# Performance work log

Hardware: AMD Instinct MI355X
Metric: run time of the kernel (lower is better)

## Reference

```python
import jax, jax.numpy as jnp
import numpy as np

FIELD_DIMS = [100000, 1000, 100, 50]
NUM_FEATURES = 12
NUM_CAT = len(FIELD_DIMS)
NUM_CONT = NUM_FEATURES - NUM_CAT
D = 32            # embed_dim
HID = [64, 32]
B, T = 1024, 200
BN_EPS = 1e-5


def setup_inputs() -> dict:
    key = jax.random.key(0)
    ks = jax.random.split(key, 32)
    # x: [B, T, F]; first NUM_CAT cols are integer category ids stored as float
    cat_cols = [jax.random.randint(ks[i], (B, T, 1), 0, FIELD_DIMS[i]).astype(jnp.float32)
                for i in range(NUM_CAT)]
    cont_cols = jax.random.normal(ks[4], (B, T, NUM_CONT), dtype=jnp.float32)
    x = jnp.concatenate(cat_cols + [cont_cols], axis=-1)
    s = 0.05
    inp = {"x": x}
    for i, fd in enumerate(FIELD_DIMS):
        inp[f"emb{i}"] = jax.random.normal(ks[5 + i], (fd, D), dtype=jnp.float32) * s
        inp[f"lin{i}"] = jax.random.normal(ks[9 + i], (fd, D), dtype=jnp.float32) * s
    # Conv1d(1, D, 1) per continuous field == per-field affine map scalar -> D
    inp["cont_w"]  = jax.random.normal(ks[13], (NUM_CONT, D), dtype=jnp.float32) * s
    inp["cont_b"]  = jax.random.normal(ks[14], (NUM_CONT, D), dtype=jnp.float32) * s
    inp["clin_w"]  = jax.random.normal(ks[15], (NUM_CONT, D), dtype=jnp.float32) * s
    inp["clin_b"]  = jax.random.normal(ks[16], (NUM_CONT, D), dtype=jnp.float32) * s
    inp["fin_bias"] = jnp.zeros((D,), dtype=jnp.float32)
    # DNN tower: kernel_size-1 Conv1d == dense over channel dim
    dims = [NUM_FEATURES * D] + HID
    for li in range(len(HID)):
        fan_in = dims[li]
        inp[f"w{li+1}"] = jax.random.normal(ks[17 + 4 * li], (HID[li], fan_in), dtype=jnp.float32) / np.sqrt(fan_in)
        inp[f"b{li+1}"] = jnp.zeros((HID[li],), dtype=jnp.float32)
        inp[f"g{li+1}"] = jnp.ones((HID[li],), dtype=jnp.float32)
        inp[f"beta{li+1}"] = jnp.zeros((HID[li],), dtype=jnp.float32)
    inp["w_out"] = jax.random.normal(ks[30], (D, HID[-1]), dtype=jnp.float32) / np.sqrt(HID[-1])
    inp["b_out"] = jnp.zeros((D,), dtype=jnp.float32)
    return inp


def _batchnorm(h, g, b):
    # training-mode BN over (batch, time), biased variance (torch default)
    mu = h.mean(axis=(0, 1))
    var = h.var(axis=(0, 1))
    return g * (h - mu) * jax.lax.rsqrt(var + BN_EPS) + b


def reference(x, emb0, emb1, emb2, emb3, lin0, lin1, lin2, lin3,
              cont_w, cont_b, clin_w, clin_b, fin_bias,
              w1, b1, g1, beta1, w2, b2, g2, beta2, w_out, b_out):
    embs = [emb0, emb1, emb2, emb3]
    lins = [lin0, lin1, lin2, lin3]
    cat_idx = x[..., :NUM_CAT].astype(jnp.int32)          # [B,T,C]
    xc = x[..., NUM_CAT:]                                  # [B,T,Nc]

    # per-field embeddings -> [B,T,F,D]
    cat_emb = jnp.stack([embs[i][cat_idx[..., i]] for i in range(NUM_CAT)], axis=2)
    cont_emb = xc[..., None] * cont_w + cont_b             # [B,T,Nc,D]
    emb_all = jnp.concatenate([cat_emb, cont_emb], axis=2)  # [B,T,F,D]

    # FM pairwise interaction (sum-of-squares trick)
    s = emb_all.sum(axis=2)                                # [B,T,D]
    interaction = 0.5 * (s * s - (emb_all * emb_all).sum(axis=2))

    # linear terms
    lin_cat = sum(lins[i][cat_idx[..., i]] for i in range(NUM_CAT))      # [B,T,D]
    lin_cont = (xc[..., None] * clin_w + clin_b).sum(axis=2)             # [B,T,D]
    linear = lin_cat + lin_cont + fin_bias

    # DNN tower (k=1 convs == dense over F*D channels); dropout omitted (eval)
    h = emb_all.reshape(B, T, NUM_FEATURES * D)
    h = jax.nn.relu(_batchnorm(h @ w1.T + b1, g1, beta1))
    h = jax.nn.relu(_batchnorm(h @ w2.T + b2, g2, beta2))
    dnn = h @ w_out.T + b_out                              # [B,T,D]

    return linear + interaction + dnn                      # [B,T,D]
```

## Files before the change

### kernel.cpp

```cpp
#include <hip/hip_runtime.h>
#include <hip/hip_bf16.h>

typedef __hip_bfloat16 bf16;

#define ROWS 204800
#define N_INV (1.0f / 204800.0f)

__device__ float g_stats[256];
__device__ bf16  g_E1_0b[100000 * 64];
__device__ float g_E1_1[1000 * 64];
__device__ float g_E1_2[100 * 64];
__device__ float g_E1_3[50 * 64];
__device__ float g_U[8 * 64];
__device__ float g_Vb[64];
__device__ bf16  g_h1p[ROWS * 64];
__device__ bf16  g_h2p[ROWS * 32];
__device__ bf16  g_fmp[ROWS * 32];

__device__ __forceinline__ int clampi(int v, int hi) {
    return v < 0 ? 0 : (v > hi ? hi : v);
}
__device__ __forceinline__ float rl_f(float v, int l) {
    return __uint_as_float((unsigned int)__builtin_amdgcn_readlane((int)__float_as_uint(v), l));
}
__device__ __forceinline__ float us2f(unsigned short u) {
    return __uint_as_float(((unsigned int)u) << 16);
}

__device__ __forceinline__ int swz8(int d) {
    return (d & ~7) | ((d & 7) ^ ((d >> 3) & 7));
}
__device__ __forceinline__ int swz4(int d) {
    return (d & ~3) | ((d & 3) ^ (((d >> 2) ^ (d >> 4)) & 3));
}

#define GLOAD16(gp, lp)                                                        \
    __builtin_amdgcn_global_load_lds(                                          \
        (const __attribute__((address_space(1))) unsigned int*)(gp),           \
        (__attribute__((address_space(3))) unsigned int*)(lp), 16, 0, 0)

__global__ __launch_bounds__(64) void precompute_kernel(
    const float* __restrict__ emb1, const float* __restrict__ emb2, const float* __restrict__ emb3,
    const float* __restrict__ cont_w, const float* __restrict__ cont_b,
    const float* __restrict__ w1, const float* __restrict__ b1)
{
    int b = blockIdx.x;
    int k = threadIdx.x;
    __shared__ float row[32];

    if (b < 1150) {
        const float* tab; float* out; int i, colOff;
        if (b < 1000)      { tab = emb1; out = g_E1_1; i = b;        colOff = 32; }
        else if (b < 1100) { tab = emb2; out = g_E1_2; i = b - 1000; colOff = 64; }
        else               { tab = emb3; out = g_E1_3; i = b - 1100; colOff = 96; }
        if (k < 32) row[k] = tab[i * 32 + k];
        __syncthreads();
        const float* wr = w1 + k * 384 + colOff;
        float acc = 0.f;
        #pragma unroll
        for (int d = 0; d < 32; ++d) acc = fmaf(row[d], wr[d], acc);
        out[i * 64 + k] = acc;
    } else {
        g_stats[k]       = 0.f;
        g_stats[k + 64]  = 0.f;
        g_stats[k + 128] = 0.f;
        g_stats[k + 192] = 0.f;

        float vb = b1[k];
        #pragma unroll
        for (int j = 0; j < 8; ++j) {
            const float* wr = w1 + k * 384 + (4 + j) * 32;
            float u = 0.f;
            #pragma unroll
            for (int d = 0; d < 32; ++d) {
                float w = wr[d];
                u  = fmaf(cont_w[j * 32 + d], w, u);
                vb = fmaf(cont_b[j * 32 + d], w, vb);
            }
            g_U[j * 64 + k] = u;
        }
        g_Vb[k] = vb;
    }
}

__global__ __launch_bounds__(256) void e10_kernel(
    const float* __restrict__ emb0, const float* __restrict__ w1)
{
    int lane = threadIdx.x & 63;
    int wv   = threadIdx.x >> 6;
    int h    = lane >> 5;

    float w1col[32];
    {
        const float4* wr = (const float4*)(w1 + lane * 384);
        #pragma unroll
        for (int q = 0; q < 8; ++q) {
            float4 v = wr[q];
            w1col[4*q+0] = v.x; w1col[4*q+1] = v.y;
            w1col[4*q+2] = v.z; w1col[4*q+3] = v.w;
        }
    }

    for (int i = blockIdx.x * 8 + wv * 2; i < 100000; i += gridDim.x * 8) {
        int iA = i, iB = i + 1;
        float e = emb0[(h ? iB : iA) * 32 + (lane & 31)];

        float a0 = 0.f, a1 = 0.f, a2 = 0.f, a3 = 0.f;
        float b0 = 0.f, b1v = 0.f, b2v = 0.f, b3 = 0.f;
        #pragma unroll
        for (int dd = 0; dd < 32; dd += 4) {
            a0  = fmaf(rl_f(e, dd + 0),      w1col[dd + 0], a0);
            a1  = fmaf(rl_f(e, dd + 1),      w1col[dd + 1], a1);
            a2  = fmaf(rl_f(e, dd + 2),      w1col[dd + 2], a2);
            a3  = fmaf(rl_f(e, dd + 3),      w1col[dd + 3], a3);
            b0  = fmaf(rl_f(e, 32 + dd + 0), w1col[dd + 0], b0);
            b1v = fmaf(rl_f(e, 32 + dd + 1), w1col[dd + 1], b1v);
            b2v = fmaf(rl_f(e, 32 + dd + 2), w1col[dd + 2], b2v);
            b3  = fmaf(rl_f(e, 32 + dd + 3), w1col[dd + 3], b3);
        }
        g_E1_0b[iA * 64 + lane] = __float2bfloat16((a0 + a1) + (a2 + a3));
        g_E1_0b[iB * 64 + lane] = __float2bfloat16((b0 + b1v) + (b2v + b3));
    }
}

__global__ __launch_bounds__(256, 4) void phase1_kernel(
    const float* __restrict__ x,
    const float* __restrict__ emb0, const float* __restrict__ lin0,
    const float* __restrict__ emb1, const float* __restrict__ lin1,
    const float* __restrict__ emb2, const float* __restrict__ lin2,
    const float* __restrict__ emb3, const float* __restrict__ lin3,
    const float* __restrict__ cont_w, const float* __restrict__ cont_b,
    const float* __restrict__ clin_w, const float* __restrict__ clin_b,
    const float* __restrict__ fin_bias)
{
    __shared__ float lsum[64], lsq[64];

    int tid  = threadIdx.x;
    int lane = tid & 63;
    int wv   = tid >> 6;
    int d    = lane & 31;
    bool lo  = lane < 32;

    if (tid < 64) { lsum[tid] = 0.f; lsq[tid] = 0.f; }
    __syncthreads();

    float uk[8];
    #pragma unroll
    for (int j = 0; j < 8; ++j) uk[j] = g_U[j * 64 + lane];
    float vbk = g_Vb[lane];

    float p1[8], p2[8], fb = 0.f;
    if (lo) {
        #pragma unroll
        for (int j = 0; j < 8; ++j) { p1[j] = cont_w[j * 32 + d]; p2[j] = cont_b[j * 32 + d]; }
    } else {
        #pragma unroll
        for (int j = 0; j < 8; ++j) { p1[j] = clin_w[j * 32 + d]; p2[j] = clin_b[j * 32 + d]; }
        fb = fin_bias[d];
    }

    const float* T0 = lo ? emb0 : lin0;
    const float* T1 = lo ? emb1 : lin1;
    const float* T2 = lo ? emb2 : lin2;
    const float* T3 = lo ? emb3 : lin3;

    int gw   = blockIdx.x * 4 + wv;
    int base = gw * 16;

    float xs[4];
    #pragma unroll
    for (int g = 0; g < 4; ++g)
        xs[g] = (lane < 48) ? x[(base + 4 * g) * 12 + lane] : 0.f;

    float ga[2][4], gb[2][4], gc[2][4], gd[2][4], t1[2][4], t2[2][4], t3[2][4];
    unsigned short e0u[2][4];

    auto issue = [&](int g, int s) {
        #pragma unroll
        for (int t = 0; t < 4; ++t) {
            int f  = t * 12;
            int i0 = clampi((int)rl_f(xs[g], f + 0), 99999);
            int i1 = clampi((int)rl_f(xs[g], f + 1), 999);
            int i2 = clampi((int)rl_f(xs[g], f + 2), 99);
            int i3 = clampi((int)rl_f(xs[g], f + 3), 49);
            ga[s][t]  = T0[i0 * 32 + d];
            gb[s][t]  = T1[i1 * 32 + d];
            gc[s][t]  = T2[i2 * 32 + d];
            gd[s][t]  = T3[i3 * 32 + d];
            e0u[s][t] = ((const unsigned short*)g_E1_0b)[i0 * 64 + lane];
            t1[s][t]  = g_E1_1[i1 * 64 + lane];
            t2[s][t]  = g_E1_2[i2 * 64 + lane];
            t3[s][t]  = g_E1_3[i3 * 64 + lane];
        }
    };

    issue(0, 0);

    float ss = 0.f, qq = 0.f;

    #pragma unroll
    for (int g = 0; g < 4; ++g) {
        int s = g & 1;
        if (g < 3) issue(g + 1, (g + 1) & 1);

        #pragma unroll
        for (int t = 0; t < 4; ++t) {
            int r  = base + 4 * g + t;
            int fo = t * 12 + 4;
            float xc[8];
            #pragma unroll
            for (int j = 0; j < 8; ++j) xc[j] = rl_f(xs[g], fo + j);

            float va = ga[s][t], vb = gb[s][t], vc = gc[s][t], vd = gd[s][t];

            float half_val;
            if (lo) {
                float s0 = va + vb, s1 = vc + vd;
                float q0 = fmaf(va, va, vb * vb);
                float q1 = fmaf(vc, vc, vd * vd);
                #pragma unroll
                for (int j = 0; j < 8; ++j) {
                    float ce = fmaf(xc[j], p1[j], p2[j]);
                    if (j & 1) { s1 += ce; q1 = fmaf(ce, ce, q1); }
                    else       { s0 += ce; q0 = fmaf(ce, ce, q0); }
                }
                float sfull = s0 + s1;
                half_val = 0.5f * (sfull * sfull - (q0 + q1));
            } else {
                float l0 = va + vb + fb, l1 = vc + vd;
                #pragma unroll
                for (int j = 0; j < 8; ++j) {
                    if (j & 1) l1 = fmaf(xc[j], p1[j], l1 + p2[j]);
                    else       l0 = fmaf(xc[j], p1[j], l0 + p2[j]);
                }
                half_val = l0 + l1;
            }
            float other = __shfl(half_val, lane | 32);
            if (lo) g_fmp[r * 32 + d] = __float2bfloat16(half_val + other);

            float h1 = ((vbk + us2f(e0u[s][t])) + (t1[s][t] + t2[s][t])) + t3[s][t];
            #pragma unroll
            for (int j = 0; j < 8; ++j) h1 = fmaf(xc[j], uk[j], h1);

            g_h1p[r * 64 + lane] = __float2bfloat16(h1);
            ss += h1;
            qq = fmaf(h1, h1, qq);
        }
    }

    atomicAdd(&lsum[lane], ss);
    atomicAdd(&lsq[lane], qq);
    __syncthreads();
    if (tid < 64) {
        atomicAdd(&g_stats[tid], lsum[tid]);
        atomicAdd(&g_stats[64 + tid], lsq[tid]);
    }
}

__global__ __launch_bounds__(256) void phase2_kernel(
    const float* __restrict__ w2, const float* __restrict__ b2,
    const float* __restrict__ g1, const float* __restrict__ beta1)
{
    __shared__ float sa[64], sc[64];
    __shared__ float ls[64];
    __shared__ uint4 hbuf[4][512];

    int tid  = threadIdx.x;
    int lane = tid & 63;
    int wv   = tid >> 6;
    size_t rowBase = (size_t)(blockIdx.x * 4 + wv) * 64;

    {
        const char* gsrc = (const char*)g_h1p + rowBase * 128;
        #pragma unroll
        for (int i = 0; i < 8; ++i) {
            int dlin = (i << 6) + lane;
            GLOAD16(gsrc + swz8(dlin) * 16, &hbuf[wv][i << 6]);
        }
    }

    if (tid < 64) {
        float mu  = g_stats[tid] * N_INV;
        float var = g_stats[64 + tid] * N_INV - mu * mu;
        float a   = g1[tid] * rsqrtf(var + 1e-5f);
        sa[tid] = a;
        sc[tid] = beta1[tid] - a * mu;
        ls[tid] = 0.f;
    }
    __syncthreads();
    asm volatile("s_waitcnt vmcnt(0)" ::: "memory");

    const uint4* lrow = hbuf[wv] + (lane << 3);
    int r7 = lane & 7;

    float acc[32];
    #pragma unroll
    for (int m = 0; m < 32; ++m) acc[m] = 0.f;

    #pragma unroll
    for (int half = 0; half < 2; ++half) {
        uint4 u[4];
        #pragma unroll
        for (int q = 0; q < 4; ++q) u[q] = lrow[(half * 4 + q) ^ r7];

        float y[32];
        #pragma unroll
        for (int q = 0; q < 4; ++q) {
            unsigned int w4[4] = {u[q].x, u[q].y, u[q].z, u[q].w};
            #pragma unroll
            for (int j = 0; j < 4; ++j) {
                int i  = q * 4 + j;
                int ch = half * 32 + 2 * i;
                float f0 = __uint_as_float(w4[j] << 16);
                float f1 = __uint_as_float(w4[j] & 0xffff0000u);
                y[2*i]     = fmaxf(0.f, fmaf(sa[ch],     f0, sc[ch]));
                y[2*i + 1] = fmaxf(0.f, fmaf(sa[ch + 1], f1, sc[ch + 1]));
            }
        }

        #pragma unroll
        for (int m = 0; m < 32; ++m) {
            const float* wr = w2 + m * 64 + half * 32;
            float a0 = 0.f, a1 = 0.f, a2 = 0.f, a3 = 0.f;
            #pragma unroll
            for (int k = 0; k < 32; k += 4) {
                a0 = fmaf(y[k + 0], wr[k + 0], a0);
                a1 = fmaf(y[k + 1], wr[k + 1], a1);
                a2 = fmaf(y[k + 2], wr[k + 2], a2);
                a3 = fmaf(y[k + 3], wr[k + 3], a3);
            }
            acc[m] += (a0 + a1) + (a2 + a3);
        }
    }

    #pragma unroll
    for (int m = 0; m < 32; ++m) acc[m] += b2[m];

    uint4 o[4];
    unsigned int* ow = (unsigned int*)o;
    #pragma unroll
    for (int i = 0; i < 16; ++i) {
        unsigned int lo16 = (unsigned int)__bfloat16_as_ushort(__float2bfloat16(acc[2*i]));
        unsigned int hi16 = (unsigned int)__bfloat16_as_ushort(__float2bfloat16(acc[2*i + 1]));
        ow[i] = lo16 | (hi16 << 16);
    }

    #pragma unroll
    for (int q = 0; q < 4; ++q) hbuf[wv][swz4((lane << 2) + q)] = o[q];
    asm volatile("s_waitcnt lgkmcnt(0)" ::: "memory");
    {
        uint4* og = (uint4*)(g_h2p + rowBase * 32);
        #pragma unroll
        for (int i = 0; i < 4; ++i) {
            int dlin = (i << 6) + lane;
            og[dlin] = hbuf[wv][swz4(dlin)];
        }
    }

    #pragma unroll
    for (int c0 = 0; c0 < 32; c0 += 8) {
        float s[8], q[8];
        #pragma unroll
        for (int j = 0; j < 8; ++j) { s[j] = acc[c0 + j]; q[j] = s[j] * s[j]; }
        #pragma unroll
        for (int off = 32; off >= 1; off >>= 1) {
            #pragma unroll
            for (int j = 0; j < 8; ++j) {
                s[j] += __shfl_xor(s[j], off);
                q[j] += __shfl_xor(q[j], off);
            }
        }
        if (lane == 0) {
            #pragma unroll
            for (int j = 0; j < 8; ++j) {
                atomicAdd(&ls[c0 + j],      s[j]);
                atomicAdd(&ls[32 + c0 + j], q[j]);
            }
        }
    }
    __syncthreads();
    if (tid < 32)       atomicAdd(&g_stats[128 + tid], ls[tid]);
    else if (tid < 64)  atomicAdd(&g_stats[160 + (tid - 32)], ls[tid]);
}

__global__ __launch_bounds__(256) void phase3_kernel(
    const float* __restrict__ w_out, const float* __restrict__ b_out,
    const float* __restrict__ g2, const float* __restrict__ beta2,
    float* __restrict__ out)
{
    __shared__ float sa[32], sc[32];
    __shared__ uint4 sbuf[4][512];

    int tid  = threadIdx.x;
    int lane = tid & 63;
    int wv   = tid >> 6;
    size_t rowBase = (size_t)(blockIdx.x * 4 + wv) * 64;

    {
        const char* gh2 = (const char*)g_h2p + rowBase * 64;
        const char* gfm = (const char*)g_fmp + rowBase * 64;
        #pragma unroll
        for (int i = 0; i < 4; ++i) {
            int dlin = (i << 6) + lane;
            GLOAD16(gh2 + swz4(dlin) * 16, &sbuf[wv][i << 6]);
        }
        #pragma unroll
        for (int i = 0; i < 4; ++i) {
            int dlin = (i << 6) + lane;
            GLOAD16(gfm + swz4(dlin) * 16, &sbuf[wv][256 + (i << 6)]);
        }
    }

    if (tid < 32) {
        float mu  = g_stats[128 + tid] * N_INV;
        float var = g_stats[160 + tid] * N_INV - mu * mu;
        float a   = g2[tid] * rsqrtf(var + 1e-5f);
        sa[tid] = a;
        sc[tid] = beta2[tid] - a * mu;
    }
    __syncthreads();
    asm volatile("s_waitcnt vmcnt(0)" ::: "memory");

    uint4 u[4], fm4[4];
    #pragma unroll
    for (int q = 0; q < 4; ++q) {
        int gidx = swz4((lane << 2) + q);
        u[q]   = sbuf[wv][gidx];
        fm4[q] = sbuf[wv][256 + gidx];
    }

    float y2[32];
    #pragma unroll
    for (int q = 0; q < 4; ++q) {
        unsigned int w4[4] = {u[q].x, u[q].y, u[q].z, u[q].w};
        #pragma unroll
        for (int j = 0; j < 4; ++j) {
            int i = q * 4 + j;
            float f0 = __uint_as_float(w4[j] << 16);
            float f1 = __uint_as_float(w4[j] & 0xffff0000u);
            y2[2*i]     = fmaxf(0.f, fmaf(sa[2*i],     f0, sc[2*i]));
            y2[2*i + 1] = fmaxf(0.f, fmaf(sa[2*i + 1], f1, sc[2*i + 1]));
        }
    }

    float fmv[32];
    {
        const unsigned int* fw = (const unsigned int*)fm4;
        #pragma unroll
        for (int i = 0; i < 16; ++i) {
            fmv[2*i]     = __uint_as_float(fw[i] << 16);
            fmv[2*i + 1] = __uint_as_float(fw[i] & 0xffff0000u);
        }
    }

    float res[32];
    #pragma unroll
    for (int dd = 0; dd < 32; ++dd) {
        const float* wr = w_out + dd * 32;
        float a0 = fmv[dd] + b_out[dd], a1 = 0.f, a2 = 0.f, a3 = 0.f;
        #pragma unroll
        for (int k = 0; k < 32; k += 4) {
            a0 = fmaf(y2[k + 0], wr[k + 0], a0);
            a1 = fmaf(y2[k + 1], wr[k + 1], a1);
            a2 = fmaf(y2[k + 2], wr[k + 2], a2);
            a3 = fmaf(y2[k + 3], wr[k + 3], a3);
        }
        res[dd] = (a0 + a1) + (a2 + a3);
    }

    #pragma unroll
    for (int q = 0; q < 8; ++q) {
        uint4 v;
        v.x = __float_as_uint(res[4*q+0]);
        v.y = __float_as_uint(res[4*q+1]);
        v.z = __float_as_uint(res[4*q+2]);
        v.w = __float_as_uint(res[4*q+3]);
        sbuf[wv][swz8((lane << 3) + q)] = v;
    }
    asm volatile("s_waitcnt lgkmcnt(0)" ::: "memory");
    {
        uint4* og = (uint4*)(out + rowBase * 32);
        #pragma unroll
        for (int i = 0; i < 8; ++i) {
            int dlin = (i << 6) + lane;
            og[dlin] = sbuf[wv][swz8(dlin)];
        }
    }
}

extern "C" void kernel_launch(void* const* d_in, const int* in_sizes, int n_in,
                              void* d_out, int out_size, void* d_ws, size_t ws_size,
                              hipStream_t stream) {
    (void)in_sizes; (void)n_in; (void)out_size; (void)d_ws; (void)ws_size;

    const float* x       = (const float*)d_in[0];
    const float* emb0    = (const float*)d_in[1];
    const float* lin0    = (const float*)d_in[2];
    const float* emb1    = (const float*)d_in[3];
    const float* lin1    = (const float*)d_in[4];
    const float* emb2    = (const float*)d_in[5];
    const float* lin2    = (const float*)d_in[6];
    const float* emb3    = (const float*)d_in[7];
    const float* lin3    = (const float*)d_in[8];
    const float* cont_w  = (const float*)d_in[9];
    const float* cont_b  = (const float*)d_in[10];
    const float* clin_w  = (const float*)d_in[11];
    const float* clin_b  = (const float*)d_in[12];
    const float* fin_bias= (const float*)d_in[13];
    const float* w1      = (const float*)d_in[14];
    const float* b1      = (const float*)d_in[15];
    const float* g1      = (const float*)d_in[16];
    const float* beta1   = (const float*)d_in[17];
    const float* w2      = (const float*)d_in[18];
    const float* b2      = (const float*)d_in[19];
    const float* g2      = (const float*)d_in[20];
    const float* beta2   = (const float*)d_in[21];
    const float* w_out   = (const float*)d_in[22];
    const float* b_out   = (const float*)d_in[23];

    float* outp = (float*)d_out;

    hipLaunchKernelGGL(precompute_kernel, dim3(1151), dim3(64), 0, stream,
                       emb1, emb2, emb3, cont_w, cont_b, w1, b1);

    hipLaunchKernelGGL(e10_kernel, dim3(1600), dim3(256), 0, stream, emb0, w1);

    hipLaunchKernelGGL(phase1_kernel, dim3(3200), dim3(256), 0, stream,
                       x, emb0, lin0, emb1, lin1, emb2, lin2, emb3, lin3,
                       cont_w, cont_b, clin_w, clin_b, fin_bias);

    hipLaunchKernelGGL(phase2_kernel, dim3(800), dim3(256), 0, stream,
                       w2, b2, g1, beta1);

    hipLaunchKernelGGL(phase3_kernel, dim3(800), dim3(256), 0, stream,
                       w_out, b_out, g2, beta2, outp);
}
```

Baseline: 334.4 us.

## Prefetch large-table gathers into LDS with deeper manually-waited pipeline

In phase1, the gathers from the 100000-row tables (emb0/lin0 and the bf16 precomputed E1_0) are moved from register loads to global_load_lds writes into per-wave LDS slots. This lets all four row groups be in flight without holding their values in registers. The remaining small-table gathers stay register double-buffered, and an explicit s_waitcnt vmcnt schedule replaces compiler-inserted waits. The aim is to hide the latency of the cold random gathers. The cost is about 24KB of extra LDS per block and a hand-counted vmcnt schedule that must stay consistent with the issued loads and stores.

```diff
diff --git a/kernel.cpp b/kernel.cpp
--- a/kernel.cpp
+++ b/kernel.cpp
@@ -38,6 +38,16 @@
     __builtin_amdgcn_global_load_lds(                                          \
         (const __attribute__((address_space(1))) unsigned int*)(gp),           \
         (__attribute__((address_space(3))) unsigned int*)(lp), 16, 0, 0)
+#define GLOAD4(gp, lp)                                                         \
+    __builtin_amdgcn_global_load_lds(                                          \
+        (const __attribute__((address_space(1))) unsigned int*)(gp),           \
+        (__attribute__((address_space(3))) unsigned int*)(lp), 4, 0, 0)
+
+#define VWAIT(n)                                                               \
+    do {                                                                       \
+        asm volatile("s_waitcnt vmcnt(" #n ")" ::: "memory");                  \
+        __builtin_amdgcn_sched_barrier(0);                                     \
+    } while (0)
 
 __global__ __launch_bounds__(64) void precompute_kernel(
     const float* __restrict__ emb1, const float* __restrict__ emb2, const float* __restrict__ emb3,
@@ -134,6 +144,8 @@
     const float* __restrict__ fin_bias)
 {
     __shared__ float lsum[64], lsq[64];
+    __shared__ float          s_va[4][4][256];
+    __shared__ unsigned short s_e0[4][4][256];
 
     int tid  = threadIdx.x;
     int lane = tid & 63;
@@ -172,37 +184,40 @@
     for (int g = 0; g < 4; ++g)
         xs[g] = (lane < 48) ? x[(base + 4 * g) * 12 + lane] : 0.f;
 
-    float ga[2][4], gb[2][4], gc[2][4], gd[2][4], t1[2][4], t2[2][4], t3[2][4];
-    unsigned short e0u[2][4];
-
-    auto issue = [&](int g, int s) {
+    float gb[2][4], gc[2][4], gd[2][4], t1[2][4], t2[2][4], t3[2][4];
+
+    auto issueL = [&](int g, int slot) {
+        #pragma unroll
+        for (int t = 0; t < 4; ++t) {
+            int i0 = clampi((int)rl_f(xs[g], t * 12), 99999);
+            GLOAD4(T0 + i0 * 32 + d, &s_va[wv][slot][t * 64]);
+            if (lane < 32) {
+                const unsigned int* pe0 =
+                    (const unsigned int*)((const unsigned short*)g_E1_0b + i0 * 64) + lane;
+                GLOAD4(pe0, &s_e0[wv][slot][t * 64]);
+            }
+        }
+    };
+
+    auto issueC = [&](int g, int s) {
         #pragma unroll
         for (int t = 0; t < 4; ++t) {
             int f  = t * 12;
-            int i0 = clampi((int)rl_f(xs[g], f + 0), 99999);
             int i1 = clampi((int)rl_f(xs[g], f + 1), 999);
             int i2 = clampi((int)rl_f(xs[g], f + 2), 99);
             int i3 = clampi((int)rl_f(xs[g], f + 3), 49);
-            ga[s][t]  = T0[i0 * 32 + d];
-            gb[s][t]  = T1[i1 * 32 + d];
-            gc[s][t]  = T2[i2 * 32 + d];
-            gd[s][t]  = T3[i3 * 32 + d];
-            e0u[s][t] = ((const unsigned short*)g_E1_0b)[i0 * 64 + lane];
-            t1[s][t]  = g_E1_1[i1 * 64 + lane];
-            t2[s][t]  = g_E1_2[i2 * 64 + lane];
-            t3[s][t]  = g_E1_3[i3 * 64 + lane];
+            gb[s][t] = T1[i1 * 32 + d];
+            gc[s][t] = T2[i2 * 32 + d];
+            gd[s][t] = T3[i3 * 32 + d];
+            t1[s][t] = g_E1_1[i1 * 64 + lane];
+            t2[s][t] = g_E1_2[i2 * 64 + lane];
+            t3[s][t] = g_E1_3[i3 * 64 + lane];
         }
     };
 
-    issue(0, 0);
-
     float ss = 0.f, qq = 0.f;
 
-    #pragma unroll
-    for (int g = 0; g < 4; ++g) {
-        int s = g & 1;
-        if (g < 3) issue(g + 1, (g + 1) & 1);
-
+    auto compute = [&](int g, int slot, int cs) {
         #pragma unroll
         for (int t = 0; t < 4; ++t) {
             int r  = base + 4 * g + t;
@@ -211,7 +226,9 @@
             #pragma unroll
             for (int j = 0; j < 8; ++j) xc[j] = rl_f(xs[g], fo + j);
 
-            float va = ga[s][t], vb = gb[s][t], vc = gc[s][t], vd = gd[s][t];
+            float va  = s_va[wv][slot][t * 64 + lane];
+            float e0f = us2f(s_e0[wv][slot][t * 64 + lane]);
+            float vb = gb[cs][t], vc = gc[cs][t], vd = gd[cs][t];
 
             float half_val;
             if (lo) {
@@ -238,7 +255,7 @@
             float other = __shfl(half_val, lane | 32);
             if (lo) g_fmp[r * 32 + d] = __float2bfloat16(half_val + other);
 
-            float h1 = ((vbk + us2f(e0u[s][t])) + (t1[s][t] + t2[s][t])) + t3[s][t];
+            float h1 = ((vbk + e0f) + (t1[cs][t] + t2[cs][t])) + t3[cs][t];
             #pragma unroll
             for (int j = 0; j < 8; ++j) h1 = fmaf(xc[j], uk[j], h1);
 
@@ -246,7 +263,26 @@
             ss += h1;
             qq = fmaf(h1, h1, qq);
         }
-    }
+    };
+
+    issueC(0, 0);
+    issueL(0, 0);
+    issueL(1, 1);
+
+    issueL(2, 2); issueC(1, 1);
+    VWAIT(16);
+    compute(0, 0, 0);
+
+    issueL(3, 3); issueC(2, 0);
+    VWAIT(16);
+    compute(1, 1, 1);
+
+    issueC(3, 1);
+    VWAIT(8);
+    compute(2, 2, 0);
+
+    VWAIT(0);
+    compute(3, 3, 1);
 
     atomicAdd(&lsum[lane], ss);
     atomicAdd(&lsq[lane], qq);
```

Result: slower. 349.3 us (+4.5%).

## Fuse five kernels into one persistent kernel with software grid barriers

Applied to the files above, without the earlier changes.

Replaces the five separate kernel launches (precompute, E1_0 table build, phase1, phase2, phase3) with a single 800-block persistent kernel. Phases are separated by an atomic-counter grid barrier, and each wave covers more work per phase. The intent is to remove launch gaps and the tail effects between kernels. In exchange, all 800 blocks must be co-resident or the barrier deadlocks, and the spin-wait barriers plus the reduced grid size for phase1 may lower parallelism and latency hiding.

```diff
diff --git a/kernel.cpp b/kernel.cpp
--- a/kernel.cpp
+++ b/kernel.cpp
@@ -5,6 +5,7 @@
 
 #define ROWS 204800
 #define N_INV (1.0f / 204800.0f)
+#define NB 800
 
 __device__ float g_stats[256];
 __device__ bf16  g_E1_0b[100000 * 64];
@@ -17,6 +18,9 @@
 __device__ bf16  g_h2p[ROWS * 32];
 __device__ bf16  g_fmp[ROWS * 32];
 
+__device__ unsigned int g_bar_cnt = 0;
+__device__ unsigned int g_bar_gen = 0;
+
 __device__ __forceinline__ int clampi(int v, int hi) {
     return v < 0 ? 0 : (v > hi ? hi : v);
 }
@@ -39,91 +43,29 @@
         (const __attribute__((address_space(1))) unsigned int*)(gp),           \
         (__attribute__((address_space(3))) unsigned int*)(lp), 16, 0, 0)
 
-__global__ __launch_bounds__(64) void precompute_kernel(
-    const float* __restrict__ emb1, const float* __restrict__ emb2, const float* __restrict__ emb3,
-    const float* __restrict__ cont_w, const float* __restrict__ cont_b,
-    const float* __restrict__ w1, const float* __restrict__ b1)
-{
-    int b = blockIdx.x;
-    int k = threadIdx.x;
-    __shared__ float row[32];
-
-    if (b < 1150) {
-        const float* tab; float* out; int i, colOff;
-        if (b < 1000)      { tab = emb1; out = g_E1_1; i = b;        colOff = 32; }
-        else if (b < 1100) { tab = emb2; out = g_E1_2; i = b - 1000; colOff = 64; }
-        else               { tab = emb3; out = g_E1_3; i = b - 1100; colOff = 96; }
-        if (k < 32) row[k] = tab[i * 32 + k];
-        __syncthreads();
-        const float* wr = w1 + k * 384 + colOff;
-        float acc = 0.f;
-        #pragma unroll
-        for (int d = 0; d < 32; ++d) acc = fmaf(row[d], wr[d], acc);
-        out[i * 64 + k] = acc;
-    } else {
-        g_stats[k]       = 0.f;
-        g_stats[k + 64]  = 0.f;
-        g_stats[k + 128] = 0.f;
-        g_stats[k + 192] = 0.f;
-
-        float vb = b1[k];
-        #pragma unroll
-        for (int j = 0; j < 8; ++j) {
-            const float* wr = w1 + k * 384 + (4 + j) * 32;
-            float u = 0.f;
-            #pragma unroll
-            for (int d = 0; d < 32; ++d) {
-                float w = wr[d];
-                u  = fmaf(cont_w[j * 32 + d], w, u);
-                vb = fmaf(cont_b[j * 32 + d], w, vb);
-            }
-            g_U[j * 64 + k] = u;
-        }
-        g_Vb[k] = vb;
+__device__ __forceinline__ void grid_sync_sw() {
+    __syncthreads();
+    if (threadIdx.x == 0) {
+        unsigned int g = __hip_atomic_load(&g_bar_gen, __ATOMIC_RELAXED,
+                                           __HIP_MEMORY_SCOPE_AGENT);
+        unsigned int t = __hip_atomic_fetch_add(&g_bar_cnt, 1u, __ATOMIC_ACQ_REL,
+                                                __HIP_MEMORY_SCOPE_AGENT);
+        if (t == NB - 1) {
+            __hip_atomic_store(&g_bar_cnt, 0u, __ATOMIC_RELAXED,
+                               __HIP_MEMORY_SCOPE_AGENT);
+            __hip_atomic_fetch_add(&g_bar_gen, 1u, __ATOMIC_ACQ_REL,
+                                   __HIP_MEMORY_SCOPE_AGENT);
+        } else {
+            while (__hip_atomic_load(&g_bar_gen, __ATOMIC_ACQUIRE,
+                                     __HIP_MEMORY_SCOPE_AGENT) == g) {
+                __builtin_amdgcn_s_sleep(2);
+            }
+        }
     }
-}
-
-__global__ __launch_bounds__(256) void e10_kernel(
-    const float* __restrict__ emb0, const float* __restrict__ w1)
-{
-    int lane = threadIdx.x & 63;
-    int wv   = threadIdx.x >> 6;
-    int h    = lane >> 5;
-
-    float w1col[32];
-    {
-        const float4* wr = (const float4*)(w1 + lane * 384);
-        #pragma unroll
-        for (int q = 0; q < 8; ++q) {
-            float4 v = wr[q];
-            w1col[4*q+0] = v.x; w1col[4*q+1] = v.y;
-            w1col[4*q+2] = v.z; w1col[4*q+3] = v.w;
-        }
-    }
-
-    for (int i = blockIdx.x * 8 + wv * 2; i < 100000; i += gridDim.x * 8) {
-        int iA = i, iB = i + 1;
-        float e = emb0[(h ? iB : iA) * 32 + (lane & 31)];
-
-        float a0 = 0.f, a1 = 0.f, a2 = 0.f, a3 = 0.f;
-        float b0 = 0.f, b1v = 0.f, b2v = 0.f, b3 = 0.f;
-        #pragma unroll
-        for (int dd = 0; dd < 32; dd += 4) {
-            a0  = fmaf(rl_f(e, dd + 0),      w1col[dd + 0], a0);
-            a1  = fmaf(rl_f(e, dd + 1),      w1col[dd + 1], a1);
-            a2  = fmaf(rl_f(e, dd + 2),      w1col[dd + 2], a2);
-            a3  = fmaf(rl_f(e, dd + 3),      w1col[dd + 3], a3);
-            b0  = fmaf(rl_f(e, 32 + dd + 0), w1col[dd + 0], b0);
-            b1v = fmaf(rl_f(e, 32 + dd + 1), w1col[dd + 1], b1v);
-            b2v = fmaf(rl_f(e, 32 + dd + 2), w1col[dd + 2], b2v);
-            b3  = fmaf(rl_f(e, 32 + dd + 3), w1col[dd + 3], b3);
-        }
-        g_E1_0b[iA * 64 + lane] = __float2bfloat16((a0 + a1) + (a2 + a3));
-        g_E1_0b[iB * 64 + lane] = __float2bfloat16((b0 + b1v) + (b2v + b3));
-    }
-}
-
-__global__ __launch_bounds__(256, 4) void phase1_kernel(
+    __syncthreads();
+}
+
+__global__ __launch_bounds__(256, 4) void fused_kernel(
     const float* __restrict__ x,
     const float* __restrict__ emb0, const float* __restrict__ lin0,
     const float* __restrict__ emb1, const float* __restrict__ lin1,
@@ -131,359 +73,421 @@
     const float* __restrict__ emb3, const float* __restrict__ lin3,
     const float* __restrict__ cont_w, const float* __restrict__ cont_b,
     const float* __restrict__ clin_w, const float* __restrict__ clin_b,
-    const float* __restrict__ fin_bias)
+    const float* __restrict__ fin_bias,
+    const float* __restrict__ w1, const float* __restrict__ b1,
+    const float* __restrict__ g1, const float* __restrict__ beta1,
+    const float* __restrict__ w2, const float* __restrict__ b2,
+    const float* __restrict__ g2, const float* __restrict__ beta2,
+    const float* __restrict__ w_out, const float* __restrict__ b_out,
+    float* __restrict__ out)
 {
-    __shared__ float lsum[64], lsq[64];
+    __shared__ uint4 big[4][512];
+    __shared__ float sa[64], sc[64], ls[64], lsum[64], lsq[64];
 
     int tid  = threadIdx.x;
     int lane = tid & 63;
     int wv   = tid >> 6;
     int d    = lane & 31;
     bool lo  = lane < 32;
+    int slot = blockIdx.x * 4 + wv;
 
     if (tid < 64) { lsum[tid] = 0.f; lsq[tid] = 0.f; }
-    __syncthreads();
-
-    float uk[8];
-    #pragma unroll
-    for (int j = 0; j < 8; ++j) uk[j] = g_U[j * 64 + lane];
-    float vbk = g_Vb[lane];
-
-    float p1[8], p2[8], fb = 0.f;
-    if (lo) {
-        #pragma unroll
-        for (int j = 0; j < 8; ++j) { p1[j] = cont_w[j * 32 + d]; p2[j] = cont_b[j * 32 + d]; }
-    } else {
-        #pragma unroll
-        for (int j = 0; j < 8; ++j) { p1[j] = clin_w[j * 32 + d]; p2[j] = clin_b[j * 32 + d]; }
-        fb = fin_bias[d];
+
+    if (slot < 1150) {
+        const float* tab; float* outp; int i, colOff;
+        if (slot < 1000)      { tab = emb1; outp = g_E1_1; i = slot;        colOff = 32; }
+        else if (slot < 1100) { tab = emb2; outp = g_E1_2; i = slot - 1000; colOff = 64; }
+        else                  { tab = emb3; outp = g_E1_3; i = slot - 1100; colOff = 96; }
+        float rv = tab[i * 32 + d];
+        const float* wr = w1 + lane * 384 + colOff;
+        float acc = 0.f;
+        #pragma unroll
+        for (int dd = 0; dd < 32; ++dd) acc = fmaf(rl_f(rv, dd), wr[dd], acc);
+        outp[i * 64 + lane] = acc;
+    } else if (slot == 1150) {
+        int k = lane;
+        g_stats[k]       = 0.f;
+        g_stats[k + 64]  = 0.f;
+        g_stats[k + 128] = 0.f;
+        g_stats[k + 192] = 0.f;
+
+        float vb = b1[k];
+        #pragma unroll
+        for (int j = 0; j < 8; ++j) {
+            const float* wr = w1 + k * 384 + (4 + j) * 32;
+            float u = 0.f;
+            #pragma unroll
+            for (int dd = 0; dd < 32; ++dd) {
+                float w = wr[dd];
+                u  = fmaf(cont_w[j * 32 + dd], w, u);
+                vb = fmaf(cont_b[j * 32 + dd], w, vb);
+            }
+            g_U[j * 64 + k] = u;
+        }
+        g_Vb[k] = vb;
     }
 
-    const float* T0 = lo ? emb0 : lin0;
-    const float* T1 = lo ? emb1 : lin1;
-    const float* T2 = lo ? emb2 : lin2;
-    const float* T3 = lo ? emb3 : lin3;
-
-    int gw   = blockIdx.x * 4 + wv;
-    int base = gw * 16;
-
-    float xs[4];
-    #pragma unroll
-    for (int g = 0; g < 4; ++g)
-        xs[g] = (lane < 48) ? x[(base + 4 * g) * 12 + lane] : 0.f;
-
-    float ga[2][4], gb[2][4], gc[2][4], gd[2][4], t1[2][4], t2[2][4], t3[2][4];
-    unsigned short e0u[2][4];
-
-    auto issue = [&](int g, int s) {
-        #pragma unroll
-        for (int t = 0; t < 4; ++t) {
-            int f  = t * 12;
-            int i0 = clampi((int)rl_f(xs[g], f + 0), 99999);
-            int i1 = clampi((int)rl_f(xs[g], f + 1), 999);
-            int i2 = clampi((int)rl_f(xs[g], f + 2), 99);
-            int i3 = clampi((int)rl_f(xs[g], f + 3), 49);
-            ga[s][t]  = T0[i0 * 32 + d];
-            gb[s][t]  = T1[i1 * 32 + d];
-            gc[s][t]  = T2[i2 * 32 + d];
-            gd[s][t]  = T3[i3 * 32 + d];
-            e0u[s][t] = ((const unsigned short*)g_E1_0b)[i0 * 64 + lane];
-            t1[s][t]  = g_E1_1[i1 * 64 + lane];
-            t2[s][t]  = g_E1_2[i2 * 64 + lane];
-            t3[s][t]  = g_E1_3[i3 * 64 + lane];
-        }
-    };
-
-    issue(0, 0);
-
-    float ss = 0.f, qq = 0.f;
-
-    #pragma unroll
-    for (int g = 0; g < 4; ++g) {
-        int s = g & 1;
-        if (g < 3) issue(g + 1, (g + 1) & 1);
-
-        #pragma unroll
-        for (int t = 0; t < 4; ++t) {
-            int r  = base + 4 * g + t;
-            int fo = t * 12 + 4;
-            float xc[8];
-            #pragma unroll
-            for (int j = 0; j < 8; ++j) xc[j] = rl_f(xs[g], fo + j);
-
-            float va = ga[s][t], vb = gb[s][t], vc = gc[s][t], vd = gd[s][t];
-
-            float half_val;
-            if (lo) {
-                float s0 = va + vb, s1 = vc + vd;
-                float q0 = fmaf(va, va, vb * vb);
-                float q1 = fmaf(vc, vc, vd * vd);
+    {
+        int h = lane >> 5;
+        float w1col[32];
+        const float4* wrv = (const float4*)(w1 + lane * 384);
+        #pragma unroll
+        for (int q = 0; q < 8; ++q) {
+            float4 v = wrv[q];
+            w1col[4*q+0] = v.x; w1col[4*q+1] = v.y;
+            w1col[4*q+2] = v.z; w1col[4*q+3] = v.w;
+        }
+        for (int i = slot * 2; i < 100000; i += 6400) {
+            int iA = i, iB = i + 1;
+            float e = emb0[(h ? iB : iA) * 32 + d];
+            float a0 = 0.f, a1 = 0.f, a2 = 0.f, a3 = 0.f;
+            float b0 = 0.f, b1v = 0.f, b2v = 0.f, b3 = 0.f;
+            #pragma unroll
+            for (int dd = 0; dd < 32; dd += 4) {
+                a0  = fmaf(rl_f(e, dd + 0),      w1col[dd + 0], a0);
+                a1  = fmaf(rl_f(e, dd + 1),      w1col[dd + 1], a1);
+                a2  = fmaf(rl_f(e, dd + 2),      w1col[dd + 2], a2);
+                a3  = fmaf(rl_f(e, dd + 3),      w1col[dd + 3], a3);
+                b0  = fmaf(rl_f(e, 32 + dd + 0), w1col[dd + 0], b0);
+                b1v = fmaf(rl_f(e, 32 + dd + 1), w1col[dd + 1], b1v);
+                b2v = fmaf(rl_f(e, 32 + dd + 2), w1col[dd + 2], b2v);
+                b3  = fmaf(rl_f(e, 32 + dd + 3), w1col[dd + 3], b3);
+            }
+            g_E1_0b[iA * 64 + lane] = __float2bfloat16((a0 + a1) + (a2 + a3));
+            g_E1_0b[iB * 64 + lane] = __float2bfloat16((b0 + b1v) + (b2v + b3));
+        }
+    }
+
+    grid_sync_sw();
+
+    {
+        float uk[8];
+        #pragma unroll
+        for (int j = 0; j < 8; ++j) uk[j] = g_U[j * 64 + lane];
+        float vbk = g_Vb[lane];
+
+        float p1[8], p2[8], fb = 0.f;
+        if (lo) {
+            #pragma unroll
+            for (int j = 0; j < 8; ++j) { p1[j] = cont_w[j * 32 + d]; p2[j] = cont_b[j * 32 + d]; }
+        } else {
+            #pragma unroll
+            for (int j = 0; j < 8; ++j) { p1[j] = clin_w[j * 32 + d]; p2[j] = clin_b[j * 32 + d]; }
+            fb = fin_bias[d];
+        }
+
+        const float* T0 = lo ? emb0 : lin0;
+        const float* T1 = lo ? emb1 : lin1;
+        const float* T2 = lo ? emb2 : lin2;
+        const float* T3 = lo ? emb3 : lin3;
+
+        float ss = 0.f, qq = 0.f;
+
+        for (int rep = 0; rep < 4; ++rep) {
+            int gw   = rep * 3200 + slot;
+            int base = gw * 16;
+
+            float xs[4];
+            #pragma unroll
+            for (int g = 0; g < 4; ++g)
+                xs[g] = (lane < 48) ? x[(base + 4 * g) * 12 + lane] : 0.f;
+
+            float ga[2][4], gb[2][4], gc[2][4], gd[2][4], t1[2][4], t2[2][4], t3[2][4];
+            unsigned short e0u[2][4];
+
+            auto issue = [&](int g, int s) {
+                #pragma unroll
+                for (int t = 0; t < 4; ++t) {
+                    int f  = t * 12;
+                    int i0 = clampi((int)rl_f(xs[g], f + 0), 99999);
+                    int i1 = clampi((int)rl_f(xs[g], f + 1), 999);
+                    int i2 = clampi((int)rl_f(xs[g], f + 2), 99);
+                    int i3 = clampi((int)rl_f(xs[g], f + 3), 49);
+                    ga[s][t]  = T0[i0 * 32 + d];
+                    gb[s][t]  = T1[i1 * 32 + d];
+                    gc[s][t]  = T2[i2 * 32 + d];
+                    gd[s][t]  = T3[i3 * 32 + d];
+                    e0u[s][t] = ((const unsigned short*)g_E1_0b)[i0 * 64 + lane];
+                    t1[s][t]  = g_E1_1[i1 * 64 + lane];
+                    t2[s][t]  = g_E1_2[i2 * 64 + lane];
+                    t3[s][t]  = g_E1_3[i3 * 64 + lane];
+                }
+            };
+
+            issue(0, 0);
+
+            #pragma unroll
+            for (int g = 0; g < 4; ++g) {
+                int s = g & 1;
+                if (g < 3) issue(g + 1, (g + 1) & 1);
+
+                #pragma unroll
+                for (int t = 0; t < 4; ++t) {
+                    int r  = base + 4 * g + t;
+                    int fo = t * 12 + 4;
+                    float xc[8];
+                    #pragma unroll
+                    for (int j = 0; j < 8; ++j) xc[j] = rl_f(xs[g], fo + j);
+
+                    float va = ga[s][t], vb = gb[s][t], vc = gc[s][t], vd = gd[s][t];
+
+                    float half_val;
+                    if (lo) {
+                        float s0 = va + vb, s1 = vc + vd;
+                        float q0 = fmaf(va, va, vb * vb);
+                        float q1 = fmaf(vc, vc, vd * vd);
+                        #pragma unroll
+                        for (int j = 0; j < 8; ++j) {
+                            float ce = fmaf(xc[j], p1[j], p2[j]);
+                            if (j & 1) { s1 += ce; q1 = fmaf(ce, ce, q1); }
+                            else       { s0 += ce; q0 = fmaf(ce, ce, q0); }
+                        }
+                        float sfull = s0 + s1;
+                        half_val = 0.5f * (sfull * sfull - (q0 + q1));
+                    } else {
+                        float l0 = va + vb + fb, l1 = vc + vd;
+                        #pragma unroll
+                        for (int j = 0; j < 8; ++j) {
+                            if (j & 1) l1 = fmaf(xc[j], p1[j], l1 + p2[j]);
+                            else       l0 = fmaf(xc[j], p1[j], l0 + p2[j]);
+                        }
+                        half_val = l0 + l1;
+                    }
+                    float other = __shfl(half_val, lane | 32);
+                    if (lo) g_fmp[r * 32 + d] = __float2bfloat16(half_val + other);
+
+                    float h1 = ((vbk + us2f(e0u[s][t])) + (t1[s][t] + t2[s][t])) + t3[s][t];
+                    #pragma unroll
+                    for (int j = 0; j < 8; ++j) h1 = fmaf(xc[j], uk[j], h1);
+
+                    g_h1p[r * 64 + lane] = __float2bfloat16(h1);
+                    ss += h1;
+                    qq = fmaf(h1, h1, qq);
+                }
+            }
+        }
+
+        atomicAdd(&lsum[lane], ss);
+        atomicAdd(&lsq[lane], qq);
+        __syncthreads();
+        if (tid < 64) {
+            atomicAdd(&g_stats[tid], lsum[tid]);
+            atomicAdd(&g_stats[64 + tid], lsq[tid]);
+        }
+    }
+
+    grid_sync_sw();
+
+    {
+        size_t rowBase = (size_t)slot * 64;
+
+        {
+            const char* gsrc = (const char*)g_h1p + rowBase * 128;
+            #pragma unroll
+            for (int i = 0; i < 8; ++i) {
+                int dlin = (i << 6) + lane;
+                GLOAD16(gsrc + swz8(dlin) * 16, &big[wv][i << 6]);
+            }
+        }
+
+        if (tid < 64) {
+            float mu  = g_stats[tid] * N_INV;
+            float var = g_stats[64 + tid] * N_INV - mu * mu;
+            float a   = g1[tid] * rsqrtf(var + 1e-5f);
+            sa[tid] = a;
+            sc[tid] = beta1[tid] - a * mu;
+            ls[tid] = 0.f;
+        }
+        __syncthreads();
+        asm volatile("s_waitcnt vmcnt(0)" ::: "memory");
+
+        const uint4* lrow = big[wv] + (lane << 3);
+        int r7 = lane & 7;
+
+        float acc[32];
+        #pragma unroll
+        for (int m = 0; m < 32; ++m) acc[m] = 0.f;
+
+        #pragma unroll
+        for (int half = 0; half < 2; ++half) {
+            uint4 u[4];
+            #pragma unroll
+            for (int q = 0; q < 4; ++q) u[q] = lrow[(half * 4 + q) ^ r7];
+
+            float y[32];
+            #pragma unroll
+            for (int q = 0; q < 4; ++q) {
+                unsigned int w4[4] = {u[q].x, u[q].y, u[q].z, u[q].w};
+                #pragma unroll
+                for (int j = 0; j < 4; ++j) {
+                    int i  = q * 4 + j;
+                    int ch = half * 32 + 2 * i;
+                    float f0 = __uint_as_float(w4[j] << 16);
+                    float f1 = __uint_as_float(w4[j] & 0xffff0000u);
+                    y[2*i]     = fmaxf(0.f, fmaf(sa[ch],     f0, sc[ch]));
+                    y[2*i + 1] = fmaxf(0.f, fmaf(sa[ch + 1], f1, sc[ch + 1]));
+                }
+            }
+
+            #pragma unroll
+            for (int m = 0; m < 32; ++m) {
+                const float* wr = w2 + m * 64 + half * 32;
+                float a0 = 0.f, a1 = 0.f, a2 = 0.f, a3 = 0.f;
+                #pragma unroll
+                for (int k = 0; k < 32; k += 4) {
+                    a0 = fmaf(y[k + 0], wr[k + 0], a0);
+                    a1 = fmaf(y[k + 1], wr[k + 1], a1);
+                    a2 = fmaf(y[k + 2], wr[k + 2], a2);
+                    a3 = fmaf(y[k + 3], wr[k + 3], a3);
+                }
+                acc[m] += (a0 + a1) + (a2 + a3);
+            }
+        }
+
+        #pragma unroll
+        for (int m = 0; m < 32; ++m) acc[m] += b2[m];
+
+        uint4 o[4];
+        unsigned int* ow = (unsigned int*)o;
+        #pragma unroll
+        for (int i = 0; i < 16; ++i) {
+            unsigned int lo16 = (unsigned int)__bfloat16_as_ushort(__float2bfloat16(acc[2*i]));
+            unsigned int hi16 = (unsigned int)__bfloat16_as_ushort(__float2bfloat16(acc[2*i + 1]));
+            ow[i] = lo16 | (hi16 << 16);
+        }
+
+        #pragma unroll
+        for (int q = 0; q < 4; ++q) big[wv][swz4((lane << 2) + q)] = o[q];
+        asm volatile("s_waitcnt lgkmcnt(0)" ::: "memory");
+        {
+            uint4* og = (uint4*)(g_h2p + rowBase * 32);
+            #pragma unroll
+            for (int i = 0; i < 4; ++i) {
+                int dlin = (i << 6) + lane;
+                og[dlin] = big[wv][swz4(dlin)];
+            }
+        }
+
+        #pragma unroll
+        for (int c0 = 0; c0 < 32; c0 += 8) {
+            float s[8], q[8];
+            #pragma unroll
+            for (int j = 0; j < 8; ++j) { s[j] = acc[c0 + j]; q[j] = s[j] * s[j]; }
+            #pragma unroll
+            for (int off = 32; off >= 1; off >>= 1) {
                 #pragma unroll
                 for (int j = 0; j < 8; ++j) {
-                    float ce = fmaf(xc[j], p1[j], p2[j]);
-                    if (j & 1) { s1 += ce; q1 = fmaf(ce, ce, q1); }
-                    else       { s0 += ce; q0 = fmaf(ce, ce, q0); }
+                    s[j] += __shfl_xor(s[j], off);
+                    q[j] += __shfl_xor(q[j], off);
                 }
-                float sfull = s0 + s1;
-                half_val = 0.5f * (sfull * sfull - (q0 + q1));
-            } else {
-                float l0 = va + vb + fb, l1 = vc + vd;
+            }
+            if (lane == 0) {
                 #pragma unroll
                 for (int j = 0; j < 8; ++j) {
-                    if (j & 1) l1 = fmaf(xc[j], p1[j], l1 + p2[j]);
-                    else       l0 = fmaf(xc[j], p1[j], l0 + p2[j]);
+                    atomicAdd(&ls[c0 + j],      s[j]);
+                    atomicAdd(&ls[32 + c0 + j], q[j]);
                 }
-                half_val = l0 + l1;
-            }
-            float other = __shfl(half_val, lane | 32);
-            if (lo) g_fmp[r * 32 + d] = __float2bfloat16(half_val + other);
-
-            float h1 = ((vbk + us2f(e0u[s][t])) + (t1[s][t] + t2[s][t])) + t3[s][t];
-            #pragma unroll
-            for (int j = 0; j < 8; ++j) h1 = fmaf(xc[j], uk[j], h1);
-
-            g_h1p[r * 64 + lane] = __float2bfloat16(h1);
-            ss += h1;
-            qq = fmaf(h1, h1, qq);
-        }
+            }
+        }
+        __syncthreads();
+        if (tid < 32)       atomicAdd(&g_stats[128 + tid], ls[tid]);
+        else if (tid < 64)  atomicAdd(&g_stats[160 + (tid - 32)], ls[tid]);
     }
 
-    atomicAdd(&lsum[lane], ss);
-    atomicAdd(&lsq[lane], qq);
-    __syncthreads();
-    if (tid < 64) {
-        atomicAdd(&g_stats[tid], lsum[tid]);
-        atomicAdd(&g_stats[64 + tid], lsq[tid]);
-    }
-}
-
-__global__ __launch_bounds__(256) void phase2_kernel(
-    const float* __restrict__ w2, const float* __restrict__ b2,
-    const float* __restrict__ g1, const float* __restrict__ beta1)
-{
-    __shared__ float sa[64], sc[64];
-    __shared__ float ls[64];
-    __shared__ uint4 hbuf[4][512];
-
-    int tid  = threadIdx.x;
-    int lane = tid & 63;
-    int wv   = tid >> 6;
-    size_t rowBase = (size_t)(blockIdx.x * 4 + wv) * 64;
+    grid_sync_sw();
 
     {
-        const char* gsrc = (const char*)g_h1p + rowBase * 128;
-        #pragma unroll
-        for (int i = 0; i < 8; ++i) {
-            int dlin = (i << 6) + lane;
-            GLOAD16(gsrc + swz8(dlin) * 16, &hbuf[wv][i << 6]);
-        }
-    }
-
-    if (tid < 64) {
-        float mu  = g_stats[tid] * N_INV;
-        float var = g_stats[64 + tid] * N_INV - mu * mu;
-        float a   = g1[tid] * rsqrtf(var + 1e-5f);
-        sa[tid] = a;
-        sc[tid] = beta1[tid] - a * mu;
-        ls[tid] = 0.f;
-    }
-    __syncthreads();
-    asm volatile("s_waitcnt vmcnt(0)" ::: "memory");
-
-    const uint4* lrow = hbuf[wv] + (lane << 3);
-    int r7 = lane & 7;
-
-    float acc[32];
-    #pragma unroll
-    for (int m = 0; m < 32; ++m) acc[m] = 0.f;
-
-    #pragma unroll
-    for (int half = 0; half < 2; ++half) {
-        uint4 u[4];
-        #pragma unroll
-        for (int q = 0; q < 4; ++q) u[q] = lrow[(half * 4 + q) ^ r7];
-
-        float y[32];
+        size_t rowBase = (size_t)slot * 64;
+
+        {
+            const char* gh2 = (const char*)g_h2p + rowBase * 64;
+            const char* gfm = (const char*)g_fmp + rowBase * 64;
+            #pragma unroll
+            for (int i = 0; i < 4; ++i) {
+                int dlin = (i << 6) + lane;
+                GLOAD16(gh2 + swz4(dlin) * 16, &big[wv][i << 6]);
+            }
+            #pragma unroll
+            for (int i = 0; i < 4; ++i) {
+                int dlin = (i << 6) + lane;
+                GLOAD16(gfm + swz4(dlin) * 16, &big[wv][256 + (i << 6)]);
+            }
+        }
+
+        if (tid < 32) {
+            float mu  = g_stats[128 + tid] * N_INV;
+            float var = g_stats[160 + tid] * N_INV - mu * mu;
+            float a   = g2[tid] * rsqrtf(var + 1e-5f);
+            sa[tid] = a;
+            sc[tid] = beta2[tid] - a * mu;
+        }
+        __syncthreads();
+        asm volatile("s_waitcnt vmcnt(0)" ::: "memory");
+
+        uint4 u[4], fm4[4];
+        #pragma unroll
+        for (int q = 0; q < 4; ++q) {
+            int gidx = swz4((lane << 2) + q);
+            u[q]   = big[wv][gidx];
+            fm4[q] = big[wv][256 + gidx];
+        }
+
+        float y2[32];
         #pragma unroll
         for (int q = 0; q < 4; ++q) {
             unsigned int w4[4] = {u[q].x, u[q].y, u[q].z, u[q].w};
             #pragma unroll
             for (int j = 0; j < 4; ++j) {
-                int i  = q * 4 + j;
-                int ch = half * 32 + 2 * i;
+                int i = q * 4 + j;
                 float f0 = __uint_as_float(w4[j] << 16);
                 float f1 = __uint_as_float(w4[j] & 0xffff0000u);
-                y[2*i]     = fmaxf(0.f, fmaf(sa[ch],     f0, sc[ch]));
-                y[2*i + 1] = fmaxf(0.f, fmaf(sa[ch + 1], f1, sc[ch + 1]));
-            }
-        }
-
-        #pragma unroll
-        for (int m = 0; m < 32; ++m) {
-            const float* wr = w2 + m * 64 + half * 32;
-            float a0 = 0.f, a1 = 0.f, a2 = 0.f, a3 = 0.f;
+                y2[2*i]     = fmaxf(0.f, fmaf(sa[2*i],     f0, sc[2*i]));
+                y2[2*i + 1] = fmaxf(0.f, fmaf(sa[2*i + 1], f1, sc[2*i + 1]));
+            }
+        }
+
+        float fmv[32];
+        {
+            const unsigned int* fw = (const unsigned int*)fm4;
+            #pragma unroll
+            for (int i = 0; i < 16; ++i) {
+                fmv[2*i]     = __uint_as_float(fw[i] << 16);
+                fmv[2*i + 1] = __uint_as_float(fw[i] & 0xffff0000u);
+            }
+        }
+
+        float res[32];
+        #pragma unroll
+        for (int dd = 0; dd < 32; ++dd) {
+            const float* wr = w_out + dd * 32;
+            float a0 = fmv[dd] + b_out[dd], a1 = 0.f, a2 = 0.f, a3 = 0.f;
             #pragma unroll
             for (int k = 0; k < 32; k += 4) {
-                a0 = fmaf(y[k + 0], wr[k + 0], a0);
-                a1 = fmaf(y[k + 1], wr[k + 1], a1);
-                a2 = fmaf(y[k + 2], wr[k + 2], a2);
-                a3 = fmaf(y[k + 3], wr[k + 3], a3);
-            }
-            acc[m] += (a0 + a1) + (a2 + a3);
-        }
-    }
-
-    #pragma unroll
-    for (int m = 0; m < 32; ++m) acc[m] += b2[m];
-
-    uint4 o[4];
-    unsigned int* ow = (unsigned int*)o;
-    #pragma unroll
-    for (int i = 0; i < 16; ++i) {
-        unsigned int lo16 = (unsigned int)__bfloat16_as_ushort(__float2bfloat16(acc[2*i]));
-        unsigned int hi16 = (unsigned int)__bfloat16_as_ushort(__float2bfloat16(acc[2*i + 1]));
-        ow[i] = lo16 | (hi16 << 16);
-    }
-
-    #pragma unroll
-    for (int q = 0; q < 4; ++q) hbuf[wv][swz4((lane << 2) + q)] = o[q];
-    asm volatile("s_waitcnt lgkmcnt(0)" ::: "memory");
-    {
-        uint4* og = (uint4*)(g_h2p + rowBase * 32);
-        #pragma unroll
-        for (int i = 0; i < 4; ++i) {
-            int dlin = (i << 6) + lane;
-            og[dlin] = hbuf[wv][swz4(dlin)];
-        }
-    }
-
-    #pragma unroll
-    for (int c0 = 0; c0 < 32; c0 += 8) {
-        float s[8], q[8];
-        #pragma unroll
-        for (int j = 0; j < 8; ++j) { s[j] = acc[c0 + j]; q[j] = s[j] * s[j]; }
-        #pragma unroll
-        for (int off = 32; off >= 1; off >>= 1) {
-            #pragma unroll
-            for (int j = 0; j < 8; ++j) {
-                s[j] += __shfl_xor(s[j], off);
-                q[j] += __shfl_xor(q[j], off);
-            }
-        }
-        if (lane == 0) {
-            #pragma unroll
-            for (int j = 0; j < 8; ++j) {
-                atomicAdd(&ls[c0 + j],      s[j]);
-                atomicAdd(&ls[32 + c0 + j], q[j]);
-            }
-        }
-    }
-    __syncthreads();
-    if (tid < 32)       atomicAdd(&g_stats[128 + tid], ls[tid]);
-    else if (tid < 64)  atomicAdd(&g_stats[160 + (tid - 32)], ls[tid]);
-}
-
-__global__ __launch_bounds__(256) void phase3_kernel(
-    const float* __restrict__ w_out, const float* __restrict__ b_out,
-    const float* __restrict__ g2, const float* __restrict__ beta2,
-    float* __restrict__ out)
-{
-    __shared__ float sa[32], sc[32];
-    __shared__ uint4 sbuf[4][512];
-
-    int tid  = threadIdx.x;
-    int lane = tid & 63;
-    int wv   = tid >> 6;
-    size_t rowBase = (size_t)(blockIdx.x * 4 + wv) * 64;
-
-    {
-        const char* gh2 = (const char*)g_h2p + rowBase * 64;
-        const char* gfm = (const char*)g_fmp + rowBase * 64;
-        #pragma unroll
-        for (int i = 0; i < 4; ++i) {
-            int dlin = (i << 6) + lane;
-            GLOAD16(gh2 + swz4(dlin) * 16, &sbuf[wv][i << 6]);
-        }
-        #pragma unroll
-        for (int i = 0; i < 4; ++i) {
-            int dlin = (i << 6) + lane;
-            GLOAD16(gfm + swz4(dlin) * 16, &sbuf[wv][256 + (i << 6)]);
-        }
-    }
-
-    if (tid < 32) {
-        float mu  = g_stats[128 + tid] * N_INV;
-        float var = g_stats[160 + tid] * N_INV - mu * mu;
-        float a   = g2[tid] * rsqrtf(var + 1e-5f);
-        sa[tid] = a;
-        sc[tid] = beta2[tid] - a * mu;
-    }
-    __syncthreads();
-    asm volatile("s_waitcnt vmcnt(0)" ::: "memory");
-
-    uint4 u[4], fm4[4];
-    #pragma unroll
-    for (int q = 0; q < 4; ++q) {
-        int gidx = swz4((lane << 2) + q);
-        u[q]   = sbuf[wv][gidx];
-        fm4[q] = sbuf[wv][256 + gidx];
-    }
-
-    float y2[32];
-    #pragma unroll
-    for (int q = 0; q < 4; ++q) {
-        unsigned int w4[4] = {u[q].x, u[q].y, u[q].z, u[q].w};
-        #pragma unroll
-        for (int j = 0; j < 4; ++j) {
-            int i = q * 4 + j;
-            float f0 = __uint_as_float(w4[j] << 16);
-            float f1 = __uint_as_float(w4[j] & 0xffff0000u);
-            y2[2*i]     = fmaxf(0.f, fmaf(sa[2*i],     f0, sc[2*i]));
-            y2[2*i + 1] = fmaxf(0.f, fmaf(sa[2*i + 1], f1, sc[2*i + 1]));
-        }
-    }
-
-    float fmv[32];
-    {
-        const unsigned int* fw = (const unsigned int*)fm4;
-        #pragma unroll
-        for (int i = 0; i < 16; ++i) {
-            fmv[2*i]     = __uint_as_float(fw[i] << 16);
-            fmv[2*i + 1] = __uint_as_float(fw[i] & 0xffff0000u);
-        }
-    }
-
-    float res[32];
-    #pragma unroll
-    for (int dd = 0; dd < 32; ++dd) {
-        const float* wr = w_out + dd * 32;
-        float a0 = fmv[dd] + b_out[dd], a1 = 0.f, a2 = 0.f, a3 = 0.f;
-        #pragma unroll
-        for (int k = 0; k < 32; k += 4) {
-            a0 = fmaf(y2[k + 0], wr[k + 0], a0);
-            a1 = fmaf(y2[k + 1], wr[k + 1], a1);
-            a2 = fmaf(y2[k + 2], wr[k + 2], a2);
-            a3 = fmaf(y2[k + 3], wr[k + 3], a3);
-        }
-        res[dd] = (a0 + a1) + (a2 + a3);
-    }
-
-    #pragma unroll
-    for (int q = 0; q < 8; ++q) {
-        uint4 v;
-        v.x = __float_as_uint(res[4*q+0]);
-        v.y = __float_as_uint(res[4*q+1]);
-        v.z = __float_as_uint(res[4*q+2]);
-        v.w = __float_as_uint(res[4*q+3]);
-        sbuf[wv][swz8((lane << 3) + q)] = v;
-    }
-    asm volatile("s_waitcnt lgkmcnt(0)" ::: "memory");
-    {
-        uint4* og = (uint4*)(out + rowBase * 32);
-        #pragma unroll
-        for (int i = 0; i < 8; ++i) {
-            int dlin = (i << 6) + lane;
-            og[dlin] = sbuf[wv][swz8(dlin)];
+                a0 = fmaf(y2[k + 0], wr[k + 0], a0);
+                a1 = fmaf(y2[k + 1], wr[k + 1], a1);
+                a2 = fmaf(y2[k + 2], wr[k + 2], a2);
+                a3 = fmaf(y2[k + 3], wr[k + 3], a3);
+            }
+            res[dd] = (a0 + a1) + (a2 + a3);
+        }
+
+        #pragma unroll
+        for (int q = 0; q < 8; ++q) {
+            uint4 v;
+            v.x = __float_as_uint(res[4*q+0]);
+            v.y = __float_as_uint(res[4*q+1]);
+            v.z = __float_as_uint(res[4*q+2]);
+            v.w = __float_as_uint(res[4*q+3]);
+            big[wv][swz8((lane << 3) + q)] = v;
+        }
+        asm volatile("s_waitcnt lgkmcnt(0)" ::: "memory");
+        {
+            uint4* og = (uint4*)(out + rowBase * 32);
+            #pragma unroll
+            for (int i = 0; i < 8; ++i) {
+                int dlin = (i << 6) + lane;
+                og[dlin] = big[wv][swz8(dlin)];
+            }
         }
     }
 }
@@ -520,18 +524,9 @@
 
     float* outp = (float*)d_out;
 
-    hipLaunchKernelGGL(precompute_kernel, dim3(1151), dim3(64), 0, stream,
-                       emb1, emb2, emb3, cont_w, cont_b, w1, b1);
-
-    hipLaunchKernelGGL(e10_kernel, dim3(1600), dim3(256), 0, stream, emb0, w1);
-
-    hipLaunchKernelGGL(phase1_kernel, dim3(3200), dim3(256), 0, stream,
+    hipLaunchKernelGGL(fused_kernel, dim3(NB), dim3(256), 0, stream,
                        x, emb0, lin0, emb1, lin1, emb2, lin2, emb3, lin3,
-                       cont_w, cont_b, clin_w, clin_b, fin_bias);
-
-    hipLaunchKernelGGL(phase2_kernel, dim3(800), dim3(256), 0, stream,
-                       w2, b2, g1, beta1);
-
-    hipLaunchKernelGGL(phase3_kernel, dim3(800), dim3(256), 0, stream,
-                       w_out, b_out, g2, beta2, outp);
-}
+                       cont_w, cont_b, clin_w, clin_b, fin_bias,
+                       w1, b1, g1, beta1, w2, b2, g2, beta2,
+                       w_out, b_out, outp);
+}
```

Result: slower. 752.3 us (+125.0%).
